# Performance work log

Measured on AMD Instinct MI355X. Metric: run time of the kernel, lower is better.

The kernel has to match this reference:

```python
import jax, jax.numpy as jnp
import numpy as np

N_QUBITS = 22


def setup_inputs() -> dict:
    n = N_QUBITS
    dim = 2 ** n
    key = jax.random.key(0)
    k1, k2, k3, k4, k5 = jax.random.split(key, 5)
    return {
        "state_real": jax.random.normal(k1, (dim,), jnp.float32),
        "state_imag": jax.random.normal(k2, (dim,), jnp.float32),
        "rabi": jax.random.uniform(k3, (1,), jnp.float32),
        "detune": jax.random.uniform(k4, (1,), jnp.float32),
        "U": jax.random.normal(k5, (n, n), jnp.float32),
        "n_qubits": n,
    }


def reference(state_real, state_imag, rabi, detune, U, n_qubits):
    """kron_sum of H_rabi (Pauli-X per qubit, weight rabi/2), diagonal detune
    (weight -detune per qubit) and diagonal pairwise interaction (triu(U,1)),
    applied to a 2**n complex state vector."""
    n = n_qubits
    dim = 2 ** n
    psi = (state_real + 1j * state_imag).astype(jnp.complex64).reshape((2,) * n)

    # parse_weights: per-qubit rabi/2 for X terms, -detune for number operators
    w_x = jnp.full((n,), rabi[0] * 0.5)
    w_d = jnp.full((n,), -detune[0])

    # sum_k (rabi/2) * X_k |psi>  : X_k flips qubit-k axis of the state tensor
    x_acc = jnp.zeros_like(psi)
    for k in range(n):  # fixed small structural loop over qubits
        x_acc = x_acc + w_x[k] * jnp.flip(psi, axis=k)

    # bit table: bits[k, b] = k-th qubit bit of basis index b (axis 0 = MSB)
    basis = jnp.arange(dim, dtype=jnp.uint32)
    shifts = jnp.arange(n - 1, -1, -1, dtype=jnp.uint32)
    bits = ((basis[None, :] >> shifts[:, None]) & 1).astype(jnp.float32)  # [n, 2**n]

    # diagonal one-body detune: sum_k w_d[k] * bit_k
    diag_one = jnp.einsum("k,kn->n", w_d, bits)
    # diagonal two-body interaction: sum_{i<j} U[i,j] * bit_i * bit_j
    Ut = jnp.triu(U, k=1)
    diag_two = jnp.sum((Ut @ bits) * bits, axis=0)

    diag = (diag_one + diag_two).reshape((2,) * n)
    out = (x_acc + diag * psi).reshape(dim)
    return jnp.stack([out.real, out.imag])  # [2, 2**n] (real, imag)
```

## Files before the change

### kernel.cpp

```cpp
#include <hip/hip_runtime.h>

#define NQ 22
#define DIM (1 << NQ)
#define TILE 2048
#define LOG_TILE 11

__global__ __launch_bounds__(256) void ryd_precompute_B(const float* __restrict__ U,
                                                        float* __restrict__ Btab) {
    int t = blockIdx.x * blockDim.x + threadIdx.x;
    __shared__ float Us[NQ * NQ];
    for (int i = threadIdx.x; i < NQ * NQ; i += blockDim.x) Us[i] = U[i];
    __syncthreads();
    float b = 0.f;
    #pragma unroll
    for (int p = 1; p <= 10; ++p) {
        if ((t >> p) & 1) {
            #pragma unroll
            for (int q = 0; q < p; ++q) {
                if ((t >> q) & 1) b += Us[(21 - p) * NQ + (21 - q)];
            }
        }
    }
    Btab[t] = b;
}

#define ACC8(a0, a1, b0, b1)                                              \
    do {                                                                  \
        ar[0] += (a0).x; ar[1] += (a0).y; ar[2] += (a0).z; ar[3] += (a0).w; \
        ar[4] += (a1).x; ar[5] += (a1).y; ar[6] += (a1).z; ar[7] += (a1).w; \
        ai[0] += (b0).x; ai[1] += (b0).y; ai[2] += (b0).z; ai[3] += (b0).w; \
        ai[4] += (b1).x; ai[5] += (b1).y; ai[6] += (b1).z; ai[7] += (b1).w; \
    } while (0)

__global__ __launch_bounds__(256) void ryd_main(
    const float* __restrict__ sr_g, const float* __restrict__ si_g,
    const float* __restrict__ rabi, const float* __restrict__ detune,
    const float* __restrict__ U, const float* __restrict__ Btab,
    float* __restrict__ out) {
    __shared__ float sr[TILE];
    __shared__ float si[TILE];
    __shared__ float AD[12];

    const int h = blockIdx.x;
    const int tid = threadIdx.x;
    const int m0 = tid << 3;
    const int base = h << LOG_TILE;

    float4 r0 = *(const float4*)(sr_g + base + m0);
    float4 r1 = *(const float4*)(sr_g + base + m0 + 4);
    float4 i0 = *(const float4*)(si_g + base + m0);
    float4 i1 = *(const float4*)(si_g + base + m0 + 4);
    *(float4*)(sr + m0) = r0;
    *(float4*)(sr + m0 + 4) = r1;
    *(float4*)(si + m0) = i0;
    *(float4*)(si + m0 + 4) = i1;

    if (tid < 11) {
        int q = tid;
        float d = 0.f;
        #pragma unroll
        for (int hp = 0; hp <= 10; ++hp)
            if ((h >> hp) & 1) d += U[(10 - hp) * NQ + (21 - q)];
        AD[q] = d;
    } else if (tid == 11) {
        float a = 0.f;
        #pragma unroll
        for (int hp = 1; hp <= 10; ++hp) {
            if ((h >> hp) & 1) {
                #pragma unroll
                for (int hq = 0; hq < hp; ++hq)
                    if ((h >> hq) & 1) a += U[(10 - hp) * NQ + (10 - hq)];
            }
        }
        AD[11] = a;
    }

    float pr[8] = {r0.x, r0.y, r0.z, r0.w, r1.x, r1.y, r1.z, r1.w};
    float pi_[8] = {i0.x, i0.y, i0.z, i0.w, i1.x, i1.y, i1.z, i1.w};

    __syncthreads();

    float ar[8], ai[8];
    #pragma unroll
    for (int e = 0; e < 8; ++e) {
        ar[e] = pr[e ^ 1] + pr[e ^ 2] + pr[e ^ 4];
        ai[e] = pi_[e ^ 1] + pi_[e ^ 2] + pi_[e ^ 4];
    }

    #pragma unroll
    for (int jj = 0; jj < 8; ++jj) {
        int pt = (tid ^ (1 << jj)) << 3;
        float4 a0 = *(const float4*)(sr + pt);
        float4 a1 = *(const float4*)(sr + pt + 4);
        float4 b0 = *(const float4*)(si + pt);
        float4 b1 = *(const float4*)(si + pt + 4);
        ACC8(a0, a1, b0, b1);
    }

    #pragma unroll
    for (int jj = 0; jj < 11; ++jj) {
        int pb = ((h ^ (1 << jj)) << LOG_TILE) + m0;
        float4 a0 = *(const float4*)(sr_g + pb);
        float4 a1 = *(const float4*)(sr_g + pb + 4);
        float4 b0 = *(const float4*)(si_g + pb);
        float4 b1 = *(const float4*)(si_g + pb + 4);
        ACC8(a0, a1, b0, b1);
    }

    const float det = detune[0];
    const float hrabi = 0.5f * rabi[0];
    float Dq0 = AD[0] - det;
    float Dq1 = AD[1] - det;
    float Dq2 = AD[2] - det;
    float diagBase = AD[11] - det * (float)__popc((unsigned)h);
    #pragma unroll
    for (int j = 0; j < 8; ++j)
        if ((tid >> j) & 1) diagBase += AD[j + 3] - det;

    float4 B0 = *(const float4*)(Btab + m0);
    float4 B1 = *(const float4*)(Btab + m0 + 4);
    float Bv[8] = {B0.x, B0.y, B0.z, B0.w, B1.x, B1.y, B1.z, B1.w};

    float orv[8], oiv[8];
    #pragma unroll
    for (int e = 0; e < 8; ++e) {
        float d = diagBase + Bv[e];
        if (e & 1) d += Dq0;
        if (e & 2) d += Dq1;
        if (e & 4) d += Dq2;
        orv[e] = hrabi * ar[e] + d * pr[e];
        oiv[e] = hrabi * ai[e] + d * pi_[e];
    }

    *(float4*)(out + base + m0)           = make_float4(orv[0], orv[1], orv[2], orv[3]);
    *(float4*)(out + base + m0 + 4)       = make_float4(orv[4], orv[5], orv[6], orv[7]);
    *(float4*)(out + DIM + base + m0)     = make_float4(oiv[0], oiv[1], oiv[2], oiv[3]);
    *(float4*)(out + DIM + base + m0 + 4) = make_float4(oiv[4], oiv[5], oiv[6], oiv[7]);
}

extern "C" void kernel_launch(void* const* d_in, const int* in_sizes, int n_in,
                              void* d_out, int out_size, void* d_ws, size_t ws_size,
                              hipStream_t stream) {
    const float* state_real = (const float*)d_in[0];
    const float* state_imag = (const float*)d_in[1];
    const float* rabi       = (const float*)d_in[2];
    const float* detune     = (const float*)d_in[3];
    const float* U          = (const float*)d_in[4];
    float* Btab = (float*)d_ws;
    float* out  = (float*)d_out;

    ryd_precompute_B<<<TILE / 256, 256, 0, stream>>>(U, Btab);
    ryd_main<<<DIM / TILE, 256, 0, stream>>>(state_real, state_imag, rabi, detune,
                                             U, Btab, out);
}
```

Measured before the change: 127.0 us.

## Prefetch neighbor tiles early, swizzle shared memory, and use nontemporal output stores

```diff
diff --git a/kernel.cpp b/kernel.cpp
--- a/kernel.cpp
+++ b/kernel.cpp
@@ -4,6 +4,8 @@
 #define DIM (1 << NQ)
 #define TILE 2048
 #define LOG_TILE 11
+
+typedef float f32x4_t __attribute__((ext_vector_type(4)));
 
 __global__ __launch_bounds__(256) void ryd_precompute_B(const float* __restrict__ U,
                                                         float* __restrict__ Btab) {
@@ -32,13 +34,15 @@
         ai[4] += (b1).x; ai[5] += (b1).y; ai[6] += (b1).z; ai[7] += (b1).w; \
     } while (0)
 
-__global__ __launch_bounds__(256) void ryd_main(
+__device__ __forceinline__ int swz(int c) { return c ^ ((c >> 3) & 1); }
+
+__global__ __launch_bounds__(256, 4) void ryd_main(
     const float* __restrict__ sr_g, const float* __restrict__ si_g,
     const float* __restrict__ rabi, const float* __restrict__ detune,
     const float* __restrict__ U, const float* __restrict__ Btab,
     float* __restrict__ out) {
-    __shared__ float sr[TILE];
-    __shared__ float si[TILE];
+    __shared__ float4 srv[TILE / 4];
+    __shared__ float4 siv[TILE / 4];
     __shared__ float AD[12];
 
     const int h = blockIdx.x;
@@ -50,10 +54,25 @@
     float4 r1 = *(const float4*)(sr_g + base + m0 + 4);
     float4 i0 = *(const float4*)(si_g + base + m0);
     float4 i1 = *(const float4*)(si_g + base + m0 + 4);
-    *(float4*)(sr + m0) = r0;
-    *(float4*)(sr + m0 + 4) = r1;
-    *(float4*)(si + m0) = i0;
-    *(float4*)(si + m0 + 4) = i1;
+
+    float4 fr[3][2], fi[3][2];
+    #pragma unroll
+    for (int j = 0; j < 3; ++j) {
+        const float* pa = sr_g + ((h ^ (1 << j)) << LOG_TILE) + m0;
+        const float* pb = si_g + ((h ^ (1 << j)) << LOG_TILE) + m0;
+        fr[j][0] = *(const float4*)pa;
+        fr[j][1] = *(const float4*)(pa + 4);
+        fi[j][0] = *(const float4*)pb;
+        fi[j][1] = *(const float4*)(pb + 4);
+    }
+
+    float4 B0 = *(const float4*)(Btab + m0);
+    float4 B1 = *(const float4*)(Btab + m0 + 4);
+
+    srv[swz(2 * tid)]     = r0;
+    srv[swz(2 * tid + 1)] = r1;
+    siv[swz(2 * tid)]     = i0;
+    siv[swz(2 * tid + 1)] = i1;
 
     if (tid < 11) {
         int q = tid;
@@ -75,7 +94,7 @@
         AD[11] = a;
     }
 
-    float pr[8] = {r0.x, r0.y, r0.z, r0.w, r1.x, r1.y, r1.z, r1.w};
+    float pr[8]  = {r0.x, r0.y, r0.z, r0.w, r1.x, r1.y, r1.z, r1.w};
     float pi_[8] = {i0.x, i0.y, i0.z, i0.w, i1.x, i1.y, i1.z, i1.w};
 
     __syncthreads();
@@ -89,22 +108,33 @@
 
     #pragma unroll
     for (int jj = 0; jj < 8; ++jj) {
-        int pt = (tid ^ (1 << jj)) << 3;
-        float4 a0 = *(const float4*)(sr + pt);
-        float4 a1 = *(const float4*)(sr + pt + 4);
-        float4 b0 = *(const float4*)(si + pt);
-        float4 b1 = *(const float4*)(si + pt + 4);
+        int p = tid ^ (1 << jj);
+        float4 a0 = srv[swz(2 * p)];
+        float4 a1 = srv[swz(2 * p + 1)];
+        float4 b0 = siv[swz(2 * p)];
+        float4 b1 = siv[swz(2 * p + 1)];
         ACC8(a0, a1, b0, b1);
     }
 
     #pragma unroll
-    for (int jj = 0; jj < 11; ++jj) {
-        int pb = ((h ^ (1 << jj)) << LOG_TILE) + m0;
-        float4 a0 = *(const float4*)(sr_g + pb);
-        float4 a1 = *(const float4*)(sr_g + pb + 4);
-        float4 b0 = *(const float4*)(si_g + pb);
-        float4 b1 = *(const float4*)(si_g + pb + 4);
+    for (int j = 0; j < 3; ++j) ACC8(fr[j][0], fr[j][1], fi[j][0], fi[j][1]);
+
+    #pragma unroll
+    for (int jj = 3; jj < 11; jj += 2) {
+        const float* pa = sr_g + ((h ^ (1 << jj)) << LOG_TILE) + m0;
+        const float* pb = si_g + ((h ^ (1 << jj)) << LOG_TILE) + m0;
+        const float* pc = sr_g + ((h ^ (2 << jj)) << LOG_TILE) + m0;
+        const float* pd = si_g + ((h ^ (2 << jj)) << LOG_TILE) + m0;
+        float4 a0 = *(const float4*)pa;
+        float4 a1 = *(const float4*)(pa + 4);
+        float4 b0 = *(const float4*)pb;
+        float4 b1 = *(const float4*)(pb + 4);
+        float4 c0 = *(const float4*)pc;
+        float4 c1 = *(const float4*)(pc + 4);
+        float4 d0 = *(const float4*)pd;
+        float4 d1 = *(const float4*)(pd + 4);
         ACC8(a0, a1, b0, b1);
+        ACC8(c0, c1, d0, d1);
     }
 
     const float det = detune[0];
@@ -117,8 +147,6 @@
     for (int j = 0; j < 8; ++j)
         if ((tid >> j) & 1) diagBase += AD[j + 3] - det;
 
-    float4 B0 = *(const float4*)(Btab + m0);
-    float4 B1 = *(const float4*)(Btab + m0 + 4);
     float Bv[8] = {B0.x, B0.y, B0.z, B0.w, B1.x, B1.y, B1.z, B1.w};
 
     float orv[8], oiv[8];
@@ -132,10 +160,14 @@
         oiv[e] = hrabi * ai[e] + d * pi_[e];
     }
 
-    *(float4*)(out + base + m0)           = make_float4(orv[0], orv[1], orv[2], orv[3]);
-    *(float4*)(out + base + m0 + 4)       = make_float4(orv[4], orv[5], orv[6], orv[7]);
-    *(float4*)(out + DIM + base + m0)     = make_float4(oiv[0], oiv[1], oiv[2], oiv[3]);
-    *(float4*)(out + DIM + base + m0 + 4) = make_float4(oiv[4], oiv[5], oiv[6], oiv[7]);
+    f32x4_t o0 = {orv[0], orv[1], orv[2], orv[3]};
+    f32x4_t o1 = {orv[4], orv[5], orv[6], orv[7]};
+    f32x4_t o2 = {oiv[0], oiv[1], oiv[2], oiv[3]};
+    f32x4_t o3 = {oiv[4], oiv[5], oiv[6], oiv[7]};
+    __builtin_nontemporal_store(o0, (f32x4_t*)(out + base + m0));
+    __builtin_nontemporal_store(o1, (f32x4_t*)(out + base + m0 + 4));
+    __builtin_nontemporal_store(o2, (f32x4_t*)(out + DIM + base + m0));
+    __builtin_nontemporal_store(o3, (f32x4_t*)(out + DIM + base + m0 + 4));
 }
 
 extern "C" void kernel_launch(void* const* d_in, const int* in_sizes, int n_in,
```

Result: faster. 123.1 us (-3.1%).
